# Optimization experiments

Measured on AMD Instinct MI355X. Metric: run time of the kernel, lower is better.

## Reference

```python
import jax, jax.numpy as jnp
import numpy as np

N, E, G, F = 100000, 3200000, 256, 15
NEG_SLOPE = 0.2


def _lin(k, fi, fo):
    s = 1.0 / np.sqrt(fi)
    return jax.random.uniform(k, (fi, fo), jnp.float32, -s, s)


def _vec(k, n, fi):
    s = 1.0 / np.sqrt(fi)
    return jax.random.uniform(k, (n,), jnp.float32, -s, s)


def setup_inputs() -> dict:
    key = jax.random.key(0)
    ks = jax.random.split(key, 40)
    inp = {}
    inp["x"] = jax.random.normal(ks[0], (N, F), jnp.float32)
    inp["edge_index"] = jax.random.randint(ks[1], (2, E), 0, N, dtype=jnp.int32)
    inp["batch"] = jnp.sort(jax.random.randint(ks[2], (N,), 0, G, dtype=jnp.int32))
    inp["xA"] = jax.random.normal(ks[3], (G, 300), jnp.float32)
    i = 4
    for l in (1, 2, 3):
        inp[f"cW{l}"] = _lin(ks[i], F, F); i += 1
        inp[f"cas{l}"] = _vec(ks[i], F, F); i += 1
        inp[f"cad{l}"] = _vec(ks[i], F, F); i += 1
        inp[f"cb{l}"] = jnp.zeros((F,), jnp.float32)
        inp[f"fW{l}"] = _lin(ks[i], F, F); i += 1
        inp[f"fb{l}"] = _vec(ks[i], F, F); i += 1
    inp["m1W"] = _lin(ks[i], 90, 90); i += 1
    inp["m1b"] = _vec(ks[i], 90, 90); i += 1
    inp["aW1"] = _lin(ks[i], 300, 300); i += 1
    inp["ab1"] = _vec(ks[i], 300, 300); i += 1
    inp["aW2"] = _lin(ks[i], 300, 300); i += 1
    inp["ab2"] = _vec(ks[i], 300, 300); i += 1
    inp["aW3"] = _lin(ks[i], 300, 300); i += 1
    inp["ab3"] = _vec(ks[i], 300, 300); i += 1
    inp["aW4"] = _lin(ks[i], 300, 45); i += 1
    inp["ab4"] = _vec(ks[i], 45, 300); i += 1
    inp["m2W"] = _lin(ks[i], 90, 1); i += 1
    inp["m2b"] = _vec(ks[i], 1, 90); i += 1
    return inp


def _gat(x, src, dst, W, a_s, a_d, b):
    """PyG GATConv (heads=1, add_self_loops handled by caller via src/dst)."""
    h = x @ W                                        # [N, F]
    e = jax.nn.leaky_relu((h @ a_s)[src] + (h @ a_d)[dst], NEG_SLOPE)  # [E+N]
    mx = jax.ops.segment_max(e, dst, num_segments=N)
    ex = jnp.exp(e - mx[dst])
    den = jax.ops.segment_sum(ex, dst, num_segments=N)
    alpha = ex / (den[dst] + 1e-16)                   # segment softmax over dst
    out = jax.ops.segment_sum(h[src] * alpha[:, None], dst, num_segments=N)
    return out + b


def reference(x, edge_index, batch, xA,
              cW1, cas1, cad1, cb1, fW1, fb1,
              cW2, cas2, cad2, cb2, fW2, fb2,
              cW3, cas3, cad3, cb3, fW3, fb3,
              m1W, m1b, aW1, ab1, aW2, ab2, aW3, ab3, aW4, ab4,
              m2W, m2b):
    loop = jnp.arange(N, dtype=edge_index.dtype)      # self loops
    src = jnp.concatenate([edge_index[0], loop])
    dst = jnp.concatenate([edge_index[1], loop])

    h = _gat(x, src, dst, cW1, cas1, cad1, cb1)
    h = jax.nn.relu(h @ fW1 + fb1)
    h = _gat(h, src, dst, cW2, cas2, cad2, cb2)
    h = jax.nn.relu(h @ fW2 + fb2)
    h = _gat(h, src, dst, cW3, cas3, cad3, cb3)
    h = h @ fW3 + fb3

    s = jax.ops.segment_sum(h, batch, num_segments=G)
    mx = jax.ops.segment_max(h, batch, num_segments=G)
    cnt = jax.ops.segment_sum(jnp.ones((N, 1), h.dtype), batch, num_segments=G)
    mean = s / jnp.maximum(cnt, 1.0)
    pooled = jnp.concatenate([s, mx, mean], axis=1)   # [G, 45]

    a = jax.nn.relu(xA @ aW1 + ab1)
    a = jax.nn.relu(a @ aW2 + ab2)
    a = jax.nn.sigmoid(a @ aW3 + ab3)
    xann = a @ aW4 + ab4                              # [G, 45]

    z = jnp.concatenate([pooled, xann], axis=1)       # [G, 90]
    z = jax.nn.relu(z @ m1W + m1b)
    z = z @ m2W + m2b
    return jax.nn.sigmoid(z)
```

## Files before the change

### kernel.cpp

```cpp
#include <hip/hip_runtime.h>
#include <hip/hip_bf16.h>
#include <math.h>

#define FDIM 15
#define FPAD 16
#define NEG_SLOPE 0.2f
#define BSH 8
#define BWID 256
#define HB_GRID 256
#define HB_BLK 1024

typedef _Float16 half_t;

__device__ __forceinline__ float leaky(float e) {
  return fmaxf(NEG_SLOPE * e, e);
}

__global__ void k_zero(int* __restrict__ p, int n) {
  int i = blockIdx.x * blockDim.x + threadIdx.x;
  if (i < n) p[i] = 0;
}

__global__ void k_bhist(const int* __restrict__ dstI, int* __restrict__ bcnt,
                        int n_tot, int n_real, int NB) {
  __shared__ int hist[512];
  int tid = threadIdx.x;
  for (int i = tid; i < NB; i += blockDim.x) hist[i] = 0;
  __syncthreads();
  int stride = gridDim.x * blockDim.x;
  for (int i = blockIdx.x * blockDim.x + tid; i < n_tot; i += stride) {
    int d = (i < n_real) ? dstI[i] : (i - n_real);
    atomicAdd(&hist[d >> BSH], 1);
  }
  __syncthreads();
  for (int i = tid; i < NB; i += blockDim.x)
    if (hist[i]) atomicAdd(&bcnt[i], hist[i]);
}

__global__ void k_bscan(const int* __restrict__ bcnt, int* __restrict__ boff,
                        int* __restrict__ bcur, int* __restrict__ rowptr,
                        int NB, int N, int total) {
  __shared__ int s[512];
  int tid = threadIdx.x;
  int v = (tid < NB) ? bcnt[tid] : 0;
  s[tid] = v;
  __syncthreads();
  for (int off = 1; off < 512; off <<= 1) {
    int add = (tid >= off) ? s[tid - off] : 0;
    __syncthreads();
    s[tid] += add;
    __syncthreads();
  }
  if (tid < NB) { int e = s[tid] - v; boff[tid] = e; bcur[tid] = e; }
  if (tid == NB - 1) boff[NB] = s[tid];
  if (tid == 0) rowptr[N] = total;
}

__global__ void k_bpart(const int* __restrict__ srcI, const int* __restrict__ dstI,
                        int* __restrict__ bcur, int* __restrict__ bbuf,
                        int n_tot, int n_real, int NB) {
  __shared__ int hist[512];
  __shared__ int base[512];
  int tid = threadIdx.x;
  for (int i = tid; i < NB; i += blockDim.x) hist[i] = 0;
  __syncthreads();
  int stride = gridDim.x * blockDim.x;
  int g0 = blockIdx.x * blockDim.x + tid;
  for (int i = g0; i < n_tot; i += stride) {
    int d = (i < n_real) ? dstI[i] : (i - n_real);
    atomicAdd(&hist[d >> BSH], 1);
  }
  __syncthreads();
  for (int i = tid; i < NB; i += blockDim.x)
    base[i] = hist[i] ? atomicAdd(&bcur[i], hist[i]) : 0;
  __syncthreads();
  for (int i = tid; i < NB; i += blockDim.x) hist[i] = 0;
  __syncthreads();
  for (int i = g0; i < n_tot; i += stride) {
    int s, d;
    if (i < n_real) { s = srcI[i]; d = dstI[i]; }
    else { s = d = i - n_real; }
    int b = d >> BSH;
    int p = base[b] + atomicAdd(&hist[b], 1);
    bbuf[p] = (s << BSH) | (d & (BWID - 1));
  }
}

__global__ void k_bbuild(const int* __restrict__ boff, const int* __restrict__ bbuf,
                         int* __restrict__ rowptr, int* __restrict__ csr, int N) {
  __shared__ int hist[BWID];
  __shared__ int sc[BWID];
  int b = blockIdx.x;
  int tid = threadIdx.x;
  int base_dst = b << BSH;
  int nd = min(BWID, N - base_dst);
  int s0 = boff[b], s1 = boff[b + 1];
  if (tid < BWID) hist[tid] = 0;
  __syncthreads();
  for (int j = s0 + tid; j < s1; j += 512)
    atomicAdd(&hist[bbuf[j] & (BWID - 1)], 1);
  __syncthreads();
  int v = 0;
  if (tid < BWID) { v = hist[tid]; sc[tid] = v; }
  __syncthreads();
  for (int off = 1; off < BWID; off <<= 1) {
    int add = 0;
    if (tid < BWID && tid >= off) add = sc[tid - off];
    __syncthreads();
    if (tid < BWID) sc[tid] += add;
    __syncthreads();
  }
  if (tid < nd) rowptr[base_dst + tid] = s0 + sc[tid] - v;
  __syncthreads();
  if (tid < BWID) hist[tid] = sc[tid] - v;
  __syncthreads();
  for (int j = s0 + tid; j < s1; j += 512) {
    int e = bbuf[j];
    int dl = e & (BWID - 1);
    int p = s0 + atomicAdd(&hist[dl], 1);
    csr[p] = (e >> BSH) << 5;
  }
}

__global__ void k_transform(const float* __restrict__ in, int ld_in,
                            const float* __restrict__ W,
                            const float* __restrict__ a_s,
                            const float* __restrict__ a_d,
                            half_t* __restrict__ hp,
                            float* __restrict__ ad_,
                            int n_nodes) {
  __shared__ float Ws[FDIM * FDIM];
  __shared__ float asv[FDIM], adv[FDIM];
  int tid = threadIdx.x;
  if (tid < FDIM * FDIM) Ws[tid] = W[tid];
  if (tid < FDIM) { asv[tid] = a_s[tid]; adv[tid] = a_d[tid]; }
  __syncthreads();
  int n = blockIdx.x * blockDim.x + tid;
  if (n >= n_nodes) return;
  float xin[FDIM];
#pragma unroll
  for (int j = 0; j < FDIM; ++j) xin[j] = in[n * ld_in + j];
  float sa = 0.f, da = 0.f;
  half_t hrow[FPAD];
#pragma unroll
  for (int o = 0; o < FDIM; ++o) {
    float acc = 0.f;
#pragma unroll
    for (int k = 0; k < FDIM; ++k) acc += xin[k] * Ws[k * FDIM + o];
    hrow[o] = (half_t)acc;
    sa += acc * asv[o];
    da += acc * adv[o];
  }
  hrow[FDIM] = (half_t)sa;
  ad_[n] = da;
  float4 w0, w1;
  __builtin_memcpy(&w0, &hrow[0], 16);
  __builtin_memcpy(&w1, &hrow[8], 16);
  float4* dst = (float4*)(hp + (size_t)n * FPAD);
  dst[0] = w0;
  dst[1] = w1;
}

__global__ void k_gat(const int* __restrict__ rowptr, const int* __restrict__ csrB,
                      const half_t* __restrict__ hp, const float* __restrict__ ad_,
                      const float* __restrict__ cb, const float* __restrict__ fW,
                      const float* __restrict__ fb,
                      const float* __restrict__ nW, const float* __restrict__ nas,
                      const float* __restrict__ nad,
                      half_t* __restrict__ hp2, float* __restrict__ ad2,
                      float* __restrict__ fout,
                      const float* __restrict__ mIn, const float* __restrict__ mW,
                      const float* __restrict__ mB, float* __restrict__ mOut,
                      int mAct, int mlpG,
                      int n_nodes, int do_relu, int fuse) {
  __shared__ float Ws[FDIM * FDIM];
  __shared__ float W2s[FDIM * FDIM];
  __shared__ float cbv[FDIM], fbv[FDIM], as2v[FDIM], ad2v[FDIM];
  __shared__ float aggT[16][16];
  __shared__ float outT[16][16];
  __shared__ float mins[304];
  int tid = threadIdx.x;

  if ((int)blockIdx.x < mlpG) {
    int g = blockIdx.x;
    for (int k = tid; k < 300; k += 256) mins[k] = mIn[(size_t)g * 300 + k];
    __syncthreads();
    int j1 = tid;
    int j2 = tid + 256;
    float a0 = 0.f, a1 = 0.f, a2 = 0.f, a3 = 0.f;
    float b0 = 0.f, b1 = 0.f, b2 = 0.f, b3 = 0.f;
    for (int k = 0; k < 300; k += 4) {
      float i0 = mins[k], i1 = mins[k + 1], i2 = mins[k + 2], i3 = mins[k + 3];
      float w0 = mW[k * 300 + j1];
      float w1 = mW[(k + 1) * 300 + j1];
      float w2 = mW[(k + 2) * 300 + j1];
      float w3 = mW[(k + 3) * 300 + j1];
      a0 += i0 * w0; a1 += i1 * w1; a2 += i2 * w2; a3 += i3 * w3;
      if (j2 < 300) {
        float v0 = mW[k * 300 + j2];
        float v1 = mW[(k + 1) * 300 + j2];
        float v2 = mW[(k + 2) * 300 + j2];
        float v3 = mW[(k + 3) * 300 + j2];
        b0 += i0 * v0; b1 += i1 * v1; b2 += i2 * v2; b3 += i3 * v3;
      }
    }
    float r1 = mB[j1] + (a0 + a1) + (a2 + a3);
    r1 = (mAct == 1) ? fmaxf(r1, 0.f) : 1.f / (1.f + expf(-r1));
    mOut[(size_t)g * 300 + j1] = r1;
    if (j2 < 300) {
      float r2 = mB[j2] + (b0 + b1) + (b2 + b3);
      r2 = (mAct == 1) ? fmaxf(r2, 0.f) : 1.f / (1.f + expf(-r2));
      mOut[(size_t)g * 300 + j2] = r2;
    }
    return;
  }

  if (tid < FDIM * FDIM) Ws[tid] = fW[tid];
  if (tid < FDIM) { cbv[tid] = cb[tid]; fbv[tid] = fb[tid]; }
  if (fuse) {
    if (tid < FDIM * FDIM) W2s[tid] = nW[tid];
    if (tid < FDIM) { as2v[tid] = nas[tid]; ad2v[tid] = nad[tid]; }
  }
  __syncthreads();
  int dl = tid >> 4;
  int f  = tid & 15;
  int d  = ((int)blockIdx.x - mlpG) * 16 + dl;
  float val = 0.f;
  if (d < n_nodes) {
    int rs = rowptr[d], re = rowptr[d + 1];
    float adv = ad_[d];
    const char* hb = (const char*)hp;
    int fo = f << 1;
    float den0 = 0.f, acc0 = 0.f, den1 = 0.f, acc1 = 0.f;
    int j = rs;
    for (; j + 7 < re; j += 8) {
      int o0 = csrB[j],     o1 = csrB[j + 1], o2 = csrB[j + 2], o3 = csrB[j + 3];
      int o4 = csrB[j + 4], o5 = csrB[j + 5], o6 = csrB[j + 6], o7 = csrB[j + 7];
      float hv0 = (float)*(const half_t*)(hb + o0 + fo);
      float hv1 = (float)*(const half_t*)(hb + o1 + fo);
      float hv2 = (float)*(const half_t*)(hb + o2 + fo);
      float hv3 = (float)*(const half_t*)(hb + o3 + fo);
      float hv4 = (float)*(const half_t*)(hb + o4 + fo);
      float hv5 = (float)*(const half_t*)(hb + o5 + fo);
      float hv6 = (float)*(const half_t*)(hb + o6 + fo);
      float hv7 = (float)*(const half_t*)(hb + o7 + fo);
      float w0 = __expf(leaky(__shfl(hv0, 15, 16) + adv));
      float w1 = __expf(leaky(__shfl(hv1, 15, 16) + adv));
      float w2 = __expf(leaky(__shfl(hv2, 15, 16) + adv));
      float w3 = __expf(leaky(__shfl(hv3, 15, 16) + adv));
      float w4 = __expf(leaky(__shfl(hv4, 15, 16) + adv));
      float w5 = __expf(leaky(__shfl(hv5, 15, 16) + adv));
      float w6 = __expf(leaky(__shfl(hv6, 15, 16) + adv));
      float w7 = __expf(leaky(__shfl(hv7, 15, 16) + adv));
      den0 += w0; acc0 += hv0 * w0;
      den1 += w1; acc1 += hv1 * w1;
      den0 += w2; acc0 += hv2 * w2;
      den1 += w3; acc1 += hv3 * w3;
      den0 += w4; acc0 += hv4 * w4;
      den1 += w5; acc1 += hv5 * w5;
      den0 += w6; acc0 += hv6 * w6;
      den1 += w7; acc1 += hv7 * w7;
    }
    for (; j < re; ++j) {
      int o0 = csrB[j];
      float hv0 = (float)*(const half_t*)(hb + o0 + fo);
      float w0 = __expf(leaky(__shfl(hv0, 15, 16) + adv));
      den0 += w0; acc0 += hv0 * w0;
    }
    val = (acc0 + acc1) / (den0 + den1 + 1e-16f);
  }
  aggT[dl][f] = (f < FDIM) ? (val + cbv[f]) : 0.f;
  __syncthreads();
  int o = f;
  float ffn = 0.f;
  if (o < FDIM) {
    ffn = fbv[o];
#pragma unroll
    for (int k = 0; k < FDIM; ++k) ffn += aggT[dl][k] * Ws[k * FDIM + o];
    if (do_relu) ffn = fmaxf(ffn, 0.f);
  }
  if (!fuse) {
    if (d < n_nodes) fout[d * FPAD + o] = (o < FDIM) ? ffn : 0.f;
    return;
  }
  outT[dl][o] = ffn;
  __syncthreads();
  if (d < n_nodes) {
    float h2 = 0.f;
    if (o < FDIM) {
#pragma unroll
      for (int k = 0; k < FDIM; ++k) h2 += outT[dl][k] * W2s[k * FDIM + o];
    }
    float pa = (o < FDIM) ? h2 * as2v[o] : 0.f;
    float pd = (o < FDIM) ? h2 * ad2v[o] : 0.f;
#pragma unroll
    for (int k = 8; k; k >>= 1) {
      pa += __shfl_xor(pa, k, 16);
      pd += __shfl_xor(pd, k, 16);
    }
    hp2[(size_t)d * FPAD + o] = (half_t)((o < FDIM) ? h2 : pa);
    if (o == 0) ad2[d] = pd;
  }
}

__device__ __forceinline__ int lowerb(const int* __restrict__ a, int n, int key) {
  int lo = 0, hi = n;
  while (lo < hi) { int mid = (lo + hi) >> 1; if (a[mid] < key) lo = mid + 1; else hi = mid; }
  return lo;
}

__global__ void k_pool(const float* __restrict__ fout, const int* __restrict__ batch,
                       float* __restrict__ pooled,
                       const float* __restrict__ acts,
                       const float* __restrict__ aW4, const float* __restrict__ ab4,
                       float* __restrict__ xann,
                       int n_nodes, int Gn) {
  __shared__ float ss[256], sm[256];
  int tid = threadIdx.x;
  if ((int)blockIdx.x < Gn) {
    int g = blockIdx.x;
    float* mins = ss;
    for (int k = tid; k < 300; k += 256) {
      if (k < 256) ss[k] = acts[(size_t)g * 300 + k];
      else sm[k - 256] = acts[(size_t)g * 300 + k];
    }
    __syncthreads();
    if (tid < 45) {
      float a0 = 0.f, a1 = 0.f, a2 = 0.f, a3 = 0.f;
      for (int k = 0; k < 300; k += 4) {
        float i0 = (k < 256) ? ss[k] : sm[k - 256];
        float i1 = (k + 1 < 256) ? ss[k + 1] : sm[k - 255];
        float i2 = (k + 2 < 256) ? ss[k + 2] : sm[k - 254];
        float i3 = (k + 3 < 256) ? ss[k + 3] : sm[k - 253];
        float w0 = aW4[k * 45 + tid];
        float w1 = aW4[(k + 1) * 45 + tid];
        float w2 = aW4[(k + 2) * 45 + tid];
        float w3 = aW4[(k + 3) * 45 + tid];
        a0 += i0 * w0; a1 += i1 * w1; a2 += i2 * w2; a3 += i3 * w3;
      }
      xann[(size_t)g * 45 + tid] = ab4[tid] + (a0 + a1) + (a2 + a3);
    }
    return;
  }
  int g = blockIdx.x - Gn;
  int s = lowerb(batch, n_nodes, g);
  int e = lowerb(batch, n_nodes, g + 1);
  int f = tid & 15;
  float sum = 0.f, mx = -INFINITY;
  for (int n = s + (tid >> 4); n < e; n += 16) {
    float v = fout[n * FPAD + f];
    sum += v;
    mx = fmaxf(mx, v);
  }
  ss[tid] = sum; sm[tid] = mx;
  __syncthreads();
  for (int step = 128; step >= 16; step >>= 1) {
    if (tid < step) { ss[tid] += ss[tid + step]; sm[tid] = fmaxf(sm[tid], sm[tid + step]); }
    __syncthreads();
  }
  if (tid < FDIM) {
    float cnt = (float)(e - s);
    float sv = ss[tid];
    pooled[g * 45 + tid] = sv;
    pooled[g * 45 + 15 + tid] = sm[tid];
    pooled[g * 45 + 30 + tid] = sv / fmaxf(cnt, 1.f);
  }
}

__global__ void k_final(const float* __restrict__ pooled, const float* __restrict__ xann,
                        const float* __restrict__ m1W, const float* __restrict__ m1b,
                        const float* __restrict__ m2W, const float* __restrict__ m2b,
                        float* __restrict__ out) {
  __shared__ float z[90];
  __shared__ float z2[90];
  __shared__ float ps[128];
  int g = blockIdx.x;
  int t = threadIdx.x;
  if (t < 45) z[t] = pooled[g * 45 + t];
  else if (t < 90) z[t] = xann[g * 45 + (t - 45)];
  __syncthreads();
  if (t < 90) {
    float a0 = 0.f, a1 = 0.f;
    for (int k = 0; k < 90; k += 2) {
      float w0 = m1W[k * 90 + t];
      float w1 = m1W[(k + 1) * 90 + t];
      a0 += z[k] * w0; a1 += z[k + 1] * w1;
    }
    z2[t] = fmaxf(m1b[t] + a0 + a1, 0.f);
  }
  __syncthreads();
  if (t < 90) ps[t] = z2[t] * m2W[t];
  else ps[t] = 0.f;
  __syncthreads();
  if (t < 64) {
    float v = ps[t] + ps[t + 64];
#pragma unroll
    for (int k2 = 32; k2; k2 >>= 1) v += __shfl_xor(v, k2, 64);
    if (t == 0) out[g] = 1.f / (1.f + expf(-(v + m2b[0])));
  }
}

extern "C" void kernel_launch(void* const* d_in, const int* in_sizes, int n_in,
                              void* d_out, int out_size, void* d_ws, size_t ws_size,
                              hipStream_t stream) {
  const float* x   = (const float*)d_in[0];
  const int* ei    = (const int*)d_in[1];
  const int* batch = (const int*)d_in[2];
  const float* xA  = (const float*)d_in[3];

  const int N = in_sizes[0] / FDIM;
  const int E = in_sizes[1] / 2;
  const int G = in_sizes[3] / 300;
  const int ET = E + N;
  const int NB = (N + BWID - 1) >> BSH;

  const int* srcI = ei;
  const int* dstI = ei + E;

  float* ws = (float*)d_ws;
  size_t layerW = (size_t)34 * N;
  size_t uSize = layerW > (size_t)ET ? layerW : (size_t)ET;
  size_t off = 0;
  int*    bbuf = (int*)(ws + off);
  half_t* hpA  = (half_t*)(ws + off);
  half_t* hpB  = (half_t*)(ws + off + (size_t)8 * N);
  float*  adA  = ws + off + (size_t)16 * N;
  float*  adB  = ws + off + (size_t)17 * N;
  float*  fout = ws + off + (size_t)18 * N;
  off += uSize;
  int*   rowptr = (int*)(ws + off); off += N + 1;
  int*   csr    = (int*)(ws + off); off += (size_t)ET;
  int*   bcnt   = (int*)(ws + off); off += 516;
  int*   boff   = (int*)(ws + off); off += 516;
  int*   bcur   = (int*)(ws + off); off += 516;
  float* pooled = ws + off; off += (size_t)G * 45;
  float* a1     = ws + off; off += (size_t)G * 300;
  float* a2     = ws + off; off += (size_t)G * 300;
  float* xann   = ws + off; off += (size_t)G * 45;

  const int B = 256;
  const int gN = (N + B - 1) / B;

  k_zero<<<(NB + B - 1) / B, B, 0, stream>>>(bcnt, NB);
  k_bhist<<<HB_GRID, HB_BLK, 0, stream>>>(dstI, bcnt, ET, E, NB);
  k_bscan<<<1, 512, 0, stream>>>(bcnt, boff, bcur, rowptr, NB, N, ET);
  k_bpart<<<HB_GRID, HB_BLK, 0, stream>>>(srcI, dstI, bcur, bbuf, ET, E, NB);
  k_bbuild<<<NB, 512, 0, stream>>>(boff, bbuf, rowptr, csr, N);

  const float* cW1  = (const float*)d_in[4];
  const float* cas1 = (const float*)d_in[5];
  const float* cad1 = (const float*)d_in[6];
  const float* cb1  = (const float*)d_in[7];
  const float* fW1  = (const float*)d_in[8];
  const float* fb1  = (const float*)d_in[9];
  const float* cW2  = (const float*)d_in[10];
  const float* cas2 = (const float*)d_in[11];
  const float* cad2 = (const float*)d_in[12];
  const float* cb2  = (const float*)d_in[13];
  const float* fW2  = (const float*)d_in[14];
  const float* fb2  = (const float*)d_in[15];
  const float* cW3  = (const float*)d_in[16];
  const float* cas3 = (const float*)d_in[17];
  const float* cad3 = (const float*)d_in[18];
  const float* cb3  = (const float*)d_in[19];
  const float* fW3  = (const float*)d_in[20];
  const float* fb3  = (const float*)d_in[21];
  const float* m1W  = (const float*)d_in[22];
  const float* m1b  = (const float*)d_in[23];
  const float* aW1  = (const float*)d_in[24];
  const float* ab1  = (const float*)d_in[25];
  const float* aW2  = (const float*)d_in[26];
  const float* ab2  = (const float*)d_in[27];
  const float* aW3  = (const float*)d_in[28];
  const float* ab3  = (const float*)d_in[29];
  const float* aW4  = (const float*)d_in[30];
  const float* ab4  = (const float*)d_in[31];
  const float* m2W  = (const float*)d_in[32];
  const float* m2b  = (const float*)d_in[33];

  const int gGat = (N + 15) / 16;
  k_transform<<<gN, B, 0, stream>>>(x, FDIM, cW1, cas1, cad1, hpA, adA, N);
  k_gat<<<gGat + G, B, 0, stream>>>(rowptr, csr, hpA, adA, cb1, fW1, fb1,
                                    cW2, cas2, cad2, hpB, adB, nullptr,
                                    xA, aW1, ab1, a1, 1, G,
                                    N, 1, 1);
  k_gat<<<gGat + G, B, 0, stream>>>(rowptr, csr, hpB, adB, cb2, fW2, fb2,
                                    cW3, cas3, cad3, hpA, adA, nullptr,
                                    a1, aW2, ab2, a2, 1, G,
                                    N, 1, 1);
  k_gat<<<gGat + G, B, 0, stream>>>(rowptr, csr, hpA, adA, cb3, fW3, fb3,
                                    nullptr, nullptr, nullptr, nullptr, nullptr, fout,
                                    a2, aW3, ab3, a1, 2, G,
                                    N, 0, 0);

  k_pool<<<2 * G, B, 0, stream>>>(fout, batch, pooled, a1, aW4, ab4, xann, N, G);

  k_final<<<G, 128, 0, stream>>>(pooled, xann, m1W, m1b, m2W, m2b, (float*)d_out);
}
```

Before: 361.8 us.

## Split CSR partition into per-block histograms and redistribute MLP riders

The bucket partition pass no longer recomputes a histogram. k_bhist2 now stores each block's histogram, and a new k_base kernel turns these into per-block scan offsets, so k_bpart2 only scatters using shared-memory counters. The dense annotation MLP layers are moved onto spare blocks of the histogram and partition kernels, shifting them earlier in the stream. This takes them off the last GAT layer and the pool kernel. The cost is an extra kernel launch plus 2x256x512 ints of histogram/base workspace. The scatter order within buckets also changes to deterministic per-block order.

```diff
diff --git a/kernel.cpp b/kernel.cpp
--- a/kernel.cpp
+++ b/kernel.cpp
@@ -21,24 +21,80 @@
   if (i < n) p[i] = 0;
 }
 
-__global__ void k_bhist(const int* __restrict__ dstI, int* __restrict__ bcnt,
-                        int n_tot, int n_real, int NB) {
+__device__ __forceinline__ void mlp_rider(int g, int tid, int nthreads,
+                                          const float* __restrict__ mIn,
+                                          const float* __restrict__ mW,
+                                          const float* __restrict__ mB,
+                                          float* __restrict__ mOut,
+                                          int Nout, int mAct,
+                                          float* mins) {
+  for (int k = tid; k < 300; k += nthreads) mins[k] = mIn[(size_t)g * 300 + k];
+  __syncthreads();
+  int j1 = tid;
+  int j2 = tid + nthreads;
+  bool p1 = (j1 < Nout), p2 = (j2 < Nout);
+  float a0 = 0.f, a1 = 0.f, a2 = 0.f, a3 = 0.f;
+  float b0 = 0.f, b1 = 0.f, b2 = 0.f, b3 = 0.f;
+  if (p1) {
+    for (int k = 0; k < 300; k += 4) {
+      float i0 = mins[k], i1 = mins[k + 1], i2 = mins[k + 2], i3 = mins[k + 3];
+      float w0 = mW[k * Nout + j1];
+      float w1 = mW[(k + 1) * Nout + j1];
+      float w2 = mW[(k + 2) * Nout + j1];
+      float w3 = mW[(k + 3) * Nout + j1];
+      a0 += i0 * w0; a1 += i1 * w1; a2 += i2 * w2; a3 += i3 * w3;
+      if (p2) {
+        float v0 = mW[k * Nout + j2];
+        float v1 = mW[(k + 1) * Nout + j2];
+        float v2 = mW[(k + 2) * Nout + j2];
+        float v3 = mW[(k + 3) * Nout + j2];
+        b0 += i0 * v0; b1 += i1 * v1; b2 += i2 * v2; b3 += i3 * v3;
+      }
+    }
+    float r1 = mB[j1] + (a0 + a1) + (a2 + a3);
+    if (mAct == 1) r1 = fmaxf(r1, 0.f);
+    else if (mAct == 2) r1 = 1.f / (1.f + expf(-r1));
+    mOut[(size_t)g * Nout + j1] = r1;
+    if (p2) {
+      float r2 = mB[j2] + (b0 + b1) + (b2 + b3);
+      if (mAct == 1) r2 = fmaxf(r2, 0.f);
+      else if (mAct == 2) r2 = 1.f / (1.f + expf(-r2));
+      mOut[(size_t)g * Nout + j2] = r2;
+    }
+  }
+}
+
+__global__ void k_bhist2(const int* __restrict__ dstI, int* __restrict__ bcnt,
+                         int* __restrict__ hists,
+                         int n_tot, int n_real, int NB,
+                         const float* __restrict__ mIn, const float* __restrict__ mW,
+                         const float* __restrict__ mB, float* __restrict__ mOut,
+                         int mNout, int mAct, int mlpG) {
   __shared__ int hist[512];
-  int tid = threadIdx.x;
+  __shared__ float mins[304];
+  int tid = threadIdx.x;
+  if ((int)blockIdx.x < mlpG) {
+    mlp_rider(blockIdx.x, tid, blockDim.x, mIn, mW, mB, mOut, mNout, mAct, mins);
+    return;
+  }
+  int bid = blockIdx.x - mlpG;
   for (int i = tid; i < NB; i += blockDim.x) hist[i] = 0;
   __syncthreads();
-  int stride = gridDim.x * blockDim.x;
-  for (int i = blockIdx.x * blockDim.x + tid; i < n_tot; i += stride) {
+  int stride = HB_GRID * blockDim.x;
+  for (int i = bid * blockDim.x + tid; i < n_tot; i += stride) {
     int d = (i < n_real) ? dstI[i] : (i - n_real);
     atomicAdd(&hist[d >> BSH], 1);
   }
   __syncthreads();
-  for (int i = tid; i < NB; i += blockDim.x)
-    if (hist[i]) atomicAdd(&bcnt[i], hist[i]);
+  for (int i = tid; i < NB; i += blockDim.x) {
+    int h = hist[i];
+    hists[bid * 512 + i] = h;
+    if (h) atomicAdd(&bcnt[i], h);
+  }
 }
 
 __global__ void k_bscan(const int* __restrict__ bcnt, int* __restrict__ boff,
-                        int* __restrict__ bcur, int* __restrict__ rowptr,
+                        int* __restrict__ rowptr,
                         int NB, int N, int total) {
   __shared__ int s[512];
   int tid = threadIdx.x;
@@ -51,37 +107,51 @@
     s[tid] += add;
     __syncthreads();
   }
-  if (tid < NB) { int e = s[tid] - v; boff[tid] = e; bcur[tid] = e; }
+  if (tid < NB) boff[tid] = s[tid] - v;
   if (tid == NB - 1) boff[NB] = s[tid];
   if (tid == 0) rowptr[N] = total;
 }
 
-__global__ void k_bpart(const int* __restrict__ srcI, const int* __restrict__ dstI,
-                        int* __restrict__ bcur, int* __restrict__ bbuf,
-                        int n_tot, int n_real, int NB) {
-  __shared__ int hist[512];
-  __shared__ int base[512];
-  int tid = threadIdx.x;
-  for (int i = tid; i < NB; i += blockDim.x) hist[i] = 0;
-  __syncthreads();
-  int stride = gridDim.x * blockDim.x;
-  int g0 = blockIdx.x * blockDim.x + tid;
-  for (int i = g0; i < n_tot; i += stride) {
-    int d = (i < n_real) ? dstI[i] : (i - n_real);
-    atomicAdd(&hist[d >> BSH], 1);
-  }
-  __syncthreads();
-  for (int i = tid; i < NB; i += blockDim.x)
-    base[i] = hist[i] ? atomicAdd(&bcur[i], hist[i]) : 0;
-  __syncthreads();
-  for (int i = tid; i < NB; i += blockDim.x) hist[i] = 0;
-  __syncthreads();
-  for (int i = g0; i < n_tot; i += stride) {
+__global__ void k_base(const int* __restrict__ hists, const int* __restrict__ boff,
+                       int* __restrict__ base, int nblk) {
+  __shared__ int s[256];
+  int b = blockIdx.x;
+  int tid = threadIdx.x;
+  int v = (tid < nblk) ? hists[tid * 512 + b] : 0;
+  s[tid] = v;
+  __syncthreads();
+  for (int off = 1; off < 256; off <<= 1) {
+    int add = (tid >= off) ? s[tid - off] : 0;
+    __syncthreads();
+    s[tid] += add;
+    __syncthreads();
+  }
+  if (tid < nblk) base[tid * 512 + b] = boff[b] + s[tid] - v;
+}
+
+__global__ void k_bpart2(const int* __restrict__ srcI, const int* __restrict__ dstI,
+                         const int* __restrict__ base, int* __restrict__ bbuf,
+                         int n_tot, int n_real, int NB,
+                         const float* __restrict__ mIn, const float* __restrict__ mW,
+                         const float* __restrict__ mB, float* __restrict__ mOut,
+                         int mNout, int mAct, int mlpG) {
+  __shared__ int cur[512];
+  __shared__ float mins[304];
+  int tid = threadIdx.x;
+  if ((int)blockIdx.x < mlpG) {
+    mlp_rider(blockIdx.x, tid, blockDim.x, mIn, mW, mB, mOut, mNout, mAct, mins);
+    return;
+  }
+  int bid = blockIdx.x - mlpG;
+  for (int i = tid; i < NB; i += blockDim.x) cur[i] = base[bid * 512 + i];
+  __syncthreads();
+  int stride = HB_GRID * blockDim.x;
+  for (int i = bid * blockDim.x + tid; i < n_tot; i += stride) {
     int s, d;
     if (i < n_real) { s = srcI[i]; d = dstI[i]; }
     else { s = d = i - n_real; }
     int b = d >> BSH;
-    int p = base[b] + atomicAdd(&hist[b], 1);
+    int p = atomicAdd(&cur[b], 1);
     bbuf[p] = (s << BSH) | (d & (BWID - 1));
   }
 }
@@ -171,7 +241,7 @@
                       float* __restrict__ fout,
                       const float* __restrict__ mIn, const float* __restrict__ mW,
                       const float* __restrict__ mB, float* __restrict__ mOut,
-                      int mAct, int mlpG,
+                      int mNout, int mAct, int mlpG,
                       int n_nodes, int do_relu, int fuse) {
   __shared__ float Ws[FDIM * FDIM];
   __shared__ float W2s[FDIM * FDIM];
@@ -182,36 +252,7 @@
   int tid = threadIdx.x;
 
   if ((int)blockIdx.x < mlpG) {
-    int g = blockIdx.x;
-    for (int k = tid; k < 300; k += 256) mins[k] = mIn[(size_t)g * 300 + k];
-    __syncthreads();
-    int j1 = tid;
-    int j2 = tid + 256;
-    float a0 = 0.f, a1 = 0.f, a2 = 0.f, a3 = 0.f;
-    float b0 = 0.f, b1 = 0.f, b2 = 0.f, b3 = 0.f;
-    for (int k = 0; k < 300; k += 4) {
-      float i0 = mins[k], i1 = mins[k + 1], i2 = mins[k + 2], i3 = mins[k + 3];
-      float w0 = mW[k * 300 + j1];
-      float w1 = mW[(k + 1) * 300 + j1];
-      float w2 = mW[(k + 2) * 300 + j1];
-      float w3 = mW[(k + 3) * 300 + j1];
-      a0 += i0 * w0; a1 += i1 * w1; a2 += i2 * w2; a3 += i3 * w3;
-      if (j2 < 300) {
-        float v0 = mW[k * 300 + j2];
-        float v1 = mW[(k + 1) * 300 + j2];
-        float v2 = mW[(k + 2) * 300 + j2];
-        float v3 = mW[(k + 3) * 300 + j2];
-        b0 += i0 * v0; b1 += i1 * v1; b2 += i2 * v2; b3 += i3 * v3;
-      }
-    }
-    float r1 = mB[j1] + (a0 + a1) + (a2 + a3);
-    r1 = (mAct == 1) ? fmaxf(r1, 0.f) : 1.f / (1.f + expf(-r1));
-    mOut[(size_t)g * 300 + j1] = r1;
-    if (j2 < 300) {
-      float r2 = mB[j2] + (b0 + b1) + (b2 + b3);
-      r2 = (mAct == 1) ? fmaxf(r2, 0.f) : 1.f / (1.f + expf(-r2));
-      mOut[(size_t)g * 300 + j2] = r2;
-    }
+    mlp_rider(blockIdx.x, tid, blockDim.x, mIn, mW, mB, mOut, mNout, mAct, mins);
     return;
   }
 
@@ -310,39 +351,10 @@
 }
 
 __global__ void k_pool(const float* __restrict__ fout, const int* __restrict__ batch,
-                       float* __restrict__ pooled,
-                       const float* __restrict__ acts,
-                       const float* __restrict__ aW4, const float* __restrict__ ab4,
-                       float* __restrict__ xann,
-                       int n_nodes, int Gn) {
+                       float* __restrict__ pooled, int n_nodes) {
   __shared__ float ss[256], sm[256];
-  int tid = threadIdx.x;
-  if ((int)blockIdx.x < Gn) {
-    int g = blockIdx.x;
-    float* mins = ss;
-    for (int k = tid; k < 300; k += 256) {
-      if (k < 256) ss[k] = acts[(size_t)g * 300 + k];
-      else sm[k - 256] = acts[(size_t)g * 300 + k];
-    }
-    __syncthreads();
-    if (tid < 45) {
-      float a0 = 0.f, a1 = 0.f, a2 = 0.f, a3 = 0.f;
-      for (int k = 0; k < 300; k += 4) {
-        float i0 = (k < 256) ? ss[k] : sm[k - 256];
-        float i1 = (k + 1 < 256) ? ss[k + 1] : sm[k - 255];
-        float i2 = (k + 2 < 256) ? ss[k + 2] : sm[k - 254];
-        float i3 = (k + 3 < 256) ? ss[k + 3] : sm[k - 253];
-        float w0 = aW4[k * 45 + tid];
-        float w1 = aW4[(k + 1) * 45 + tid];
-        float w2 = aW4[(k + 2) * 45 + tid];
-        float w3 = aW4[(k + 3) * 45 + tid];
-        a0 += i0 * w0; a1 += i1 * w1; a2 += i2 * w2; a3 += i3 * w3;
-      }
-      xann[(size_t)g * 45 + tid] = ab4[tid] + (a0 + a1) + (a2 + a3);
-    }
-    return;
-  }
-  int g = blockIdx.x - Gn;
+  int g = blockIdx.x;
+  int tid = threadIdx.x;
   int s = lowerb(batch, n_nodes, g);
   int e = lowerb(batch, n_nodes, g + 1);
   int f = tid & 15;
@@ -432,7 +444,8 @@
   int*   csr    = (int*)(ws + off); off += (size_t)ET;
   int*   bcnt   = (int*)(ws + off); off += 516;
   int*   boff   = (int*)(ws + off); off += 516;
-  int*   bcur   = (int*)(ws + off); off += 516;
+  int*   hists  = (int*)(ws + off); off += 256 * 512;
+  int*   base   = (int*)(ws + off); off += 256 * 512;
   float* pooled = ws + off; off += (size_t)G * 45;
   float* a1     = ws + off; off += (size_t)G * 300;
   float* a2     = ws + off; off += (size_t)G * 300;
@@ -440,12 +453,6 @@
 
   const int B = 256;
   const int gN = (N + B - 1) / B;
-
-  k_zero<<<(NB + B - 1) / B, B, 0, stream>>>(bcnt, NB);
-  k_bhist<<<HB_GRID, HB_BLK, 0, stream>>>(dstI, bcnt, ET, E, NB);
-  k_bscan<<<1, 512, 0, stream>>>(bcnt, boff, bcur, rowptr, NB, N, ET);
-  k_bpart<<<HB_GRID, HB_BLK, 0, stream>>>(srcI, dstI, bcur, bbuf, ET, E, NB);
-  k_bbuild<<<NB, 512, 0, stream>>>(boff, bbuf, rowptr, csr, N);
 
   const float* cW1  = (const float*)d_in[4];
   const float* cas1 = (const float*)d_in[5];
@@ -478,22 +485,31 @@
   const float* m2W  = (const float*)d_in[32];
   const float* m2b  = (const float*)d_in[33];
 
+  k_zero<<<(NB + B - 1) / B, B, 0, stream>>>(bcnt, NB);
+  k_bhist2<<<HB_GRID + G, HB_BLK, 0, stream>>>(dstI, bcnt, hists, ET, E, NB,
+                                               xA, aW1, ab1, a1, 300, 1, G);
+  k_bscan<<<1, 512, 0, stream>>>(bcnt, boff, rowptr, NB, N, ET);
+  k_base<<<NB, 256, 0, stream>>>(hists, boff, base, HB_GRID);
+  k_bpart2<<<HB_GRID + G, HB_BLK, 0, stream>>>(srcI, dstI, base, bbuf, ET, E, NB,
+                                               a1, aW2, ab2, a2, 300, 1, G);
+  k_bbuild<<<NB, 512, 0, stream>>>(boff, bbuf, rowptr, csr, N);
+
   const int gGat = (N + 15) / 16;
   k_transform<<<gN, B, 0, stream>>>(x, FDIM, cW1, cas1, cad1, hpA, adA, N);
   k_gat<<<gGat + G, B, 0, stream>>>(rowptr, csr, hpA, adA, cb1, fW1, fb1,
                                     cW2, cas2, cad2, hpB, adB, nullptr,
-                                    xA, aW1, ab1, a1, 1, G,
+                                    a2, aW3, ab3, a1, 300, 2, G,
                                     N, 1, 1);
   k_gat<<<gGat + G, B, 0, stream>>>(rowptr, csr, hpB, adB, cb2, fW2, fb2,
                                     cW3, cas3, cad3, hpA, adA, nullptr,
-                                    a1, aW2, ab2, a2, 1, G,
+                                    a1, aW4, ab4, xann, 45, 0, G,
                                     N, 1, 1);
-  k_gat<<<gGat + G, B, 0, stream>>>(rowptr, csr, hpA, adA, cb3, fW3, fb3,
-                                    nullptr, nullptr, nullptr, nullptr, nullptr, fout,
-                                    a2, aW3, ab3, a1, 2, G,
-                                    N, 0, 0);
-
-  k_pool<<<2 * G, B, 0, stream>>>(fout, batch, pooled, a1, aW4, ab4, xann, N, G);
+  k_gat<<<gGat, B, 0, stream>>>(rowptr, csr, hpA, adA, cb3, fW3, fb3,
+                                nullptr, nullptr, nullptr, nullptr, nullptr, fout,
+                                nullptr, nullptr, nullptr, nullptr, 0, 0, 0,
+                                N, 0, 0);
+
+  k_pool<<<G, B, 0, stream>>>(fout, batch, pooled, N);
 
   k_final<<<G, 128, 0, stream>>>(pooled, xann, m1W, m1b, m2W, m2b, (float*)d_out);
 }
```

New measurement: 382.8 us. 1.06x slower.
